# Optimization experiments

Measured on AMD Instinct MI355X. Metric: run time of the kernel, lower is better.

Reference implementation:

```python
import jax, jax.numpy as jnp
import numpy as np

B, S, D, H, DH = 8, 1024, 768, 12, 64
INIT_STD = 0.02
IGNORE = -100000.0


def setup_inputs() -> dict:
    key = jax.random.key(0)
    ks = jax.random.split(key, 5)
    return {
        "normalized_resid_pre": jax.random.normal(ks[0], (B, S, D), dtype=jnp.float32),
        "W_Q": jax.random.normal(ks[1], (H, D, DH), dtype=jnp.float32) * INIT_STD,
        "b_Q": jnp.zeros((H, DH), dtype=jnp.float32),
        "W_K": jax.random.normal(ks[2], (H, D, DH), dtype=jnp.float32) * INIT_STD,
        "b_K": jnp.zeros((H, DH), dtype=jnp.float32),
        "W_V": jax.random.normal(ks[3], (H, D, DH), dtype=jnp.float32) * INIT_STD,
        "b_V": jnp.zeros((H, DH), dtype=jnp.float32),
        "W_O": jax.random.normal(ks[4], (H, DH, D), dtype=jnp.float32) * INIT_STD,
        "b_O": jnp.zeros((D,), dtype=jnp.float32),
    }


def reference(normalized_resid_pre, W_Q, b_Q, W_K, b_K, W_V, b_V, W_O, b_O):
    x = normalized_resid_pre  # [B,S,D]
    q = jnp.einsum('bsd,hde->bshe', x, W_Q) + b_Q  # [B,S,H,DH]
    k = jnp.einsum('bsd,hde->bshe', x, W_K) + b_K
    v = jnp.einsum('bsd,hde->bshe', x, W_V) + b_V
    scores = jnp.einsum('bqhe,bkhe->bhqk', q, k) / jnp.sqrt(jnp.float32(DH))
    causal = jnp.triu(jnp.ones((S, S), dtype=bool), k=1)  # True above diagonal
    scores = jnp.where(causal, jnp.float32(IGNORE), scores)
    pattern = jax.nn.softmax(scores, axis=-1)  # [B,H,S,S]
    z = jnp.einsum('bhqk,bkhe->bqhe', pattern, v)  # [B,S,H,DH]
    attn_out = jnp.einsum('bqhe,hed->bqd', z, W_O) + b_O  # [B,S,D]
    return attn_out
```

## Files before the change

kernel.cpp:

```cpp
#include <hip/hip_runtime.h>
#include <hip/hip_bf16.h>
#include <stdint.h>

#define BB 8
#define SS 1024
#define DD 768
#define HH 12
#define DHH 64
#define BS (BB*SS)
#define NQKV (3*HH*DHH)

typedef __attribute__((ext_vector_type(8))) short bf16x8;
typedef __attribute__((ext_vector_type(4))) float f32x4;
typedef __attribute__((ext_vector_type(4))) unsigned int u32x4;

typedef const __attribute__((address_space(1))) unsigned int gu32;
typedef __attribute__((address_space(3))) unsigned int lu32;

static __device__ __forceinline__ unsigned short f2bf(float f) {
    union { float f; unsigned int u; } v; v.f = f;
    unsigned int u = v.u;
    unsigned int r = (u + 0x7fffu + ((u >> 16) & 1u)) >> 16;
    return (unsigned short)r;
}

static __device__ __forceinline__ unsigned int cvt_pk_bf16(float lo, float hi) {
    unsigned int r;
    asm("v_cvt_pk_bf16_f32 %0, %1, %2" : "=v"(r) : "v"(lo), "v"(hi));
    return r;
}


__global__ void k_f32_to_bf16(const float* __restrict__ in, unsigned short* __restrict__ out, int n) {
    int i = (blockIdx.x * 256 + threadIdx.x) * 4;
    if (i + 3 < n) {
        float4 v = *reinterpret_cast<const float4*>(in + i);
        ushort4 o;
        o.x = f2bf(v.x); o.y = f2bf(v.y); o.z = f2bf(v.z); o.w = f2bf(v.w);
        *reinterpret_cast<ushort4*>(out + i) = o;
    } else {
        for (; i < n; ++i) out[i] = f2bf(in[i]);
    }
}

__global__ void k_transpose_wqkv(const float* __restrict__ wq, const float* __restrict__ wk,
                                 const float* __restrict__ wv, unsigned short* __restrict__ wt) {
    __shared__ float tl[64][65];
    int rt = blockIdx.x;
    int z = blockIdx.y;
    int mat = z / 12, h = z - mat * 12;
    const float* src = ((mat == 0) ? wq : (mat == 1) ? wk : wv) + (size_t)h * 768 * 64;
    int d0 = rt * 64;
    int t = threadIdx.x;
    int row = t >> 4, c4 = (t & 15) * 4;
    #pragma unroll
    for (int p = 0; p < 4; ++p) {
        int d = p * 16 + row;
        float4 v = *reinterpret_cast<const float4*>(&src[(size_t)(d0 + d) * 64 + c4]);
        tl[d][c4 + 0] = v.x; tl[d][c4 + 1] = v.y; tl[d][c4 + 2] = v.z; tl[d][c4 + 3] = v.w;
    }
    __syncthreads();
    unsigned short* dstb = wt + ((size_t)(mat * 768 + h * 64)) * 768;
    #pragma unroll
    for (int p = 0; p < 4; ++p) {
        int e = p * 16 + row;
        ushort4 o;
        o.x = f2bf(tl[c4 + 0][e]); o.y = f2bf(tl[c4 + 1][e]);
        o.z = f2bf(tl[c4 + 2][e]); o.w = f2bf(tl[c4 + 3][e]);
        *reinterpret_cast<ushort4*>(&dstb[(size_t)e * 768 + d0 + c4]) = o;
    }
}

__global__ void k_transpose_wo(const float* __restrict__ wo, unsigned short* __restrict__ wot) {
    __shared__ float tl[64][65];
    int r0 = blockIdx.x * 64;
    int c0 = blockIdx.y * 64;
    int t = threadIdx.x;
    int row = t >> 4, c4 = (t & 15) * 4;
    #pragma unroll
    for (int p = 0; p < 4; ++p) {
        int r = p * 16 + row;
        float4 v = *reinterpret_cast<const float4*>(&wo[(size_t)(r0 + r) * 768 + c0 + c4]);
        tl[r][c4 + 0] = v.x; tl[r][c4 + 1] = v.y; tl[r][c4 + 2] = v.z; tl[r][c4 + 3] = v.w;
    }
    __syncthreads();
    #pragma unroll
    for (int p = 0; p < 4; ++p) {
        int c = p * 16 + row;
        ushort4 o;
        o.x = f2bf(tl[c4 + 0][c]); o.y = f2bf(tl[c4 + 1][c]);
        o.z = f2bf(tl[c4 + 2][c]); o.w = f2bf(tl[c4 + 3][c]);
        *reinterpret_cast<ushort4*>(&wot[(size_t)(c0 + c) * 768 + r0 + c4]) = o;
    }
}

__global__ void k_transpose_v(const unsigned short* __restrict__ vb, unsigned short* __restrict__ vtb) {
    __shared__ unsigned short tl[64][68];
    int s0 = blockIdx.x * 64;
    int bh = blockIdx.y;
    const unsigned short* src = vb + (size_t)bh * SS * DHH;
    unsigned short* dst = vtb + (size_t)bh * DHH * SS;
    int t = threadIdx.x;
    #pragma unroll
    for (int i = 0; i < 16; ++i) {
        int idx = t + i * 256;
        int sl = idx >> 6, e = idx & 63;
        tl[sl][e] = src[(size_t)(s0 + sl) * DHH + e];
    }
    __syncthreads();
    #pragma unroll
    for (int i = 0; i < 16; ++i) {
        int idx = t + i * 256;
        int e = idx >> 6, sl = idx & 63;
        dst[(size_t)e * SS + s0 + sl] = tl[sl][e];
    }
}


__launch_bounds__(256)
__global__ void k_gemm_qkv(const unsigned short* __restrict__ xb,
                           const unsigned short* __restrict__ wt,
                           const float* __restrict__ bq, const float* __restrict__ bk,
                           const float* __restrict__ bv,
                           unsigned short* __restrict__ qb,
                           unsigned short* __restrict__ kb,
                           unsigned short* __restrict__ vb) {
    __shared__ unsigned short As[128 * 32];
    __shared__ unsigned short Bs[128 * 32];
    int r0 = blockIdx.x * 128;
    int c0 = blockIdx.y * 128;
    int t = threadIdx.x;
    int w = t >> 6, l = t & 63;
    int lr = l & 15, lg = l >> 4;
    int wr = w >> 1, wc = w & 1;
    int srow = l >> 2, sko = (l & 3) * 8;

    f32x4 acc[4][4] = {};
    for (int k0 = 0; k0 < DD; k0 += 32) {
        __syncthreads();
        #pragma unroll
        for (int c = 0; c < 2; ++c) {
            int seg = w * 2 + c;
            int row = seg * 16 + srow;
            __builtin_amdgcn_global_load_lds(
                (gu32*)(xb + (size_t)(r0 + row) * DD + k0 + sko),
                (lu32*)&As[seg * 512], 16, 0, 0);
            __builtin_amdgcn_global_load_lds(
                (gu32*)(wt + (size_t)(c0 + row) * DD + k0 + sko),
                (lu32*)&Bs[seg * 512], 16, 0, 0);
        }
        __syncthreads();
        bf16x8 af[4], bfr[4];
        #pragma unroll
        for (int m = 0; m < 4; ++m)
            af[m] = *reinterpret_cast<const bf16x8*>(&As[(wr * 64 + m * 16 + lr) * 32 + lg * 8]);
        #pragma unroll
        for (int n = 0; n < 4; ++n)
            bfr[n] = *reinterpret_cast<const bf16x8*>(&Bs[(wc * 64 + n * 16 + lr) * 32 + lg * 8]);
        #pragma unroll
        for (int m = 0; m < 4; ++m)
            #pragma unroll
            for (int n = 0; n < 4; ++n)
                acc[m][n] = __builtin_amdgcn_mfma_f32_16x16x32_bf16(af[m], bfr[n], acc[m][n], 0, 0, 0);
    }
    #pragma unroll
    for (int n = 0; n < 4; ++n) {
        int c = c0 + wc * 64 + n * 16 + lr;
        int mat = c / 768;
        int within = c - mat * 768;
        int h = within >> 6, e = within & 63;
        const float* bptr = (mat == 0) ? bq : (mat == 1) ? bk : bv;
        float bias = bptr[within];
        unsigned short* dst = (mat == 0) ? qb : (mat == 1) ? kb : vb;
        #pragma unroll
        for (int m = 0; m < 4; ++m) {
            #pragma unroll
            for (int i = 0; i < 4; ++i) {
                int r = r0 + wr * 64 + m * 16 + lg * 4 + i;
                int b_ = r >> 10, s_ = r & 1023;
                dst[(((size_t)(b_ * HH + h)) * SS + s_) * DHH + e] = f2bf(acc[m][n][i] + bias);
            }
        }
    }
}


#define PW 34

__launch_bounds__(256, 3)
__global__ void k_attn(const unsigned short* __restrict__ qb,
                       const unsigned short* __restrict__ kb,
                       const unsigned short* __restrict__ vtb,
                       unsigned short* __restrict__ zb) {
    __shared__ unsigned short Ks[2][64 * 64];
    __shared__ unsigned short Vs[2][64 * 64];
    __shared__ unsigned int Pl[4][16 * PW];
    int id = blockIdx.x;
    int p = id / 96;
    int bh = id - p * 96;
    int qi = 15 - p;
    int q0 = qi * 64;

    int t = threadIdx.x, w = t >> 6, l = t & 63;
    int lr = l & 15, lg = l >> 4;
    const unsigned short* Qh = qb + (size_t)bh * SS * DHH;
    const unsigned short* Kh = kb + (size_t)bh * SS * DHH;
    const unsigned short* Vt = vtb + (size_t)bh * DHH * SS;
    int b_ = bh / HH, h = bh - b_ * HH;
    unsigned int* Pw = &Pl[w][0];

    int sr8 = l >> 3;
    int sc = ((l & 7) ^ sr8) * 8;

    auto STAGE = [&](int buf, int kbase) {
        #pragma unroll
        for (int c = 0; c < 2; ++c) {
            int seg = w * 2 + c;
            int row = seg * 8 + sr8;
            __builtin_amdgcn_global_load_lds(
                (gu32*)(Kh + (size_t)(kbase + row) * DHH + sc),
                (lu32*)&Ks[buf][seg * 512], 16, 0, 0);
            __builtin_amdgcn_global_load_lds(
                (gu32*)(Vt + (size_t)row * SS + kbase + sc),
                (lu32*)&Vs[buf][seg * 512], 16, 0, 0);
        }
    };

    int qabs = q0 + w * 16 + lr;
    STAGE(0, 0);
    bf16x8 qf[2];
    qf[0] = *reinterpret_cast<const bf16x8*>(Qh + (size_t)qabs * DHH + lg * 8);
    qf[1] = *reinterpret_cast<const bf16x8*>(Qh + (size_t)qabs * DHH + 32 + lg * 8);

    float m_r = -3.0e38f, l_r = 0.f;
    f32x4 zacc[4] = {};
    __syncthreads();

    for (int kt = 0; kt <= qi; ++kt) {
        int k0 = kt * 64;
        int cur = kt & 1;
        if (kt < qi) STAGE(cur ^ 1, k0 + 64);

        f32x4 sac[4] = {};
        #pragma unroll
        for (int ks = 0; ks < 2; ++ks) {
            #pragma unroll
            for (int ct = 0; ct < 4; ++ct) {
                bf16x8 kfr = *reinterpret_cast<const bf16x8*>(
                    &Ks[cur][(ct * 16 + lr) * 64 + (((ks * 4 + lg) ^ (lr & 7)) * 8)]);
                sac[ct] = __builtin_amdgcn_mfma_f32_16x16x32_bf16(kfr, qf[ks], sac[ct], 0, 0, 0);
            }
        }
        bool diag = (kt == qi);
        float sv[4][4];
        float pm = -3.0e38f;
        #pragma unroll
        for (int ct = 0; ct < 4; ++ct) {
            #pragma unroll
            for (int i = 0; i < 4; ++i) {
                float x = sac[ct][i] * 0.125f;
                if (diag) {
                    int kabs = k0 + ct * 16 + lg * 4 + i;
                    if (kabs > qabs) x = -3.0e38f;
                }
                sv[ct][i] = x;
                pm = fmaxf(pm, x);
            }
        }
        pm = fmaxf(pm, __shfl_xor(pm, 16));
        pm = fmaxf(pm, __shfl_xor(pm, 32));

        if (!__all(pm <= m_r + 8.f)) {
            float mn = fmaxf(m_r, pm);
            float alpha = __expf(m_r - mn);
            m_r = mn;
            l_r *= alpha;
            float aC[4];
            #pragma unroll
            for (int i = 0; i < 4; ++i) aC[i] = __shfl(alpha, lg * 4 + i);
            #pragma unroll
            for (int et = 0; et < 4; ++et)
                #pragma unroll
                for (int i = 0; i < 4; ++i) zacc[et][i] *= aC[i];
        }

        float ps = 0.f;
        #pragma unroll
        for (int ct = 0; ct < 4; ++ct) {
            float p0 = __expf(sv[ct][0] - m_r);
            float p1 = __expf(sv[ct][1] - m_r);
            float p2 = __expf(sv[ct][2] - m_r);
            float p3 = __expf(sv[ct][3] - m_r);
            ps += (p0 + p1) + (p2 + p3);
            unsigned int pk0 = cvt_pk_bf16(p0, p1);
            unsigned int pk1 = cvt_pk_bf16(p2, p3);
            *reinterpret_cast<uint2*>(&Pw[lr * PW + ct * 8 + lg * 2]) = make_uint2(pk0, pk1);
        }
        ps += __shfl_xor(ps, 16);
        ps += __shfl_xor(ps, 32);
        l_r += ps;

        #pragma unroll
        for (int ks = 0; ks < 2; ++ks) {
            bf16x8 pa = *reinterpret_cast<const bf16x8*>(&Pw[lr * PW + ks * 16 + lg * 4]);
            #pragma unroll
            for (int et = 0; et < 4; ++et) {
                bf16x8 vf = *reinterpret_cast<const bf16x8*>(
                    &Vs[cur][(et * 16 + lr) * 64 + (((ks * 4 + lg) ^ (lr & 7)) * 8)]);
                zacc[et] = __builtin_amdgcn_mfma_f32_16x16x32_bf16(pa, vf, zacc[et], 0, 0, 0);
            }
        }
        __syncthreads();
    }

    float lC[4];
    #pragma unroll
    for (int i = 0; i < 4; ++i) lC[i] = __shfl(l_r, lg * 4 + i);
    #pragma unroll
    for (int et = 0; et < 4; ++et) {
        #pragma unroll
        for (int i = 0; i < 4; ++i) {
            int r = q0 + w * 16 + lg * 4 + i;
            float z = zacc[et][i] / lC[i];
            zb[((size_t)(b_ * SS + r)) * DD + h * DHH + et * 16 + lr] = f2bf(z);
        }
    }
}


__launch_bounds__(256)
__global__ void k_gemm_out(const unsigned short* __restrict__ zb,
                           const unsigned short* __restrict__ wot,
                           const float* __restrict__ bo,
                           float* __restrict__ out) {
    __shared__ unsigned short As[128 * 32];
    __shared__ unsigned short Bs[128 * 32];
    int r0 = blockIdx.x * 128;
    int c0 = blockIdx.y * 128;
    int t = threadIdx.x;
    int w = t >> 6, l = t & 63;
    int lr = l & 15, lg = l >> 4;
    int wr = w >> 1, wc = w & 1;
    int srow = l >> 2, sko = (l & 3) * 8;

    f32x4 acc[4][4] = {};
    for (int k0 = 0; k0 < DD; k0 += 32) {
        __syncthreads();
        #pragma unroll
        for (int c = 0; c < 2; ++c) {
            int seg = w * 2 + c;
            int row = seg * 16 + srow;
            __builtin_amdgcn_global_load_lds(
                (gu32*)(zb + (size_t)(r0 + row) * DD + k0 + sko),
                (lu32*)&As[seg * 512], 16, 0, 0);
            __builtin_amdgcn_global_load_lds(
                (gu32*)(wot + (size_t)(c0 + row) * DD + k0 + sko),
                (lu32*)&Bs[seg * 512], 16, 0, 0);
        }
        __syncthreads();
        bf16x8 af[4], bfr[4];
        #pragma unroll
        for (int m = 0; m < 4; ++m)
            af[m] = *reinterpret_cast<const bf16x8*>(&As[(wr * 64 + m * 16 + lr) * 32 + lg * 8]);
        #pragma unroll
        for (int n = 0; n < 4; ++n)
            bfr[n] = *reinterpret_cast<const bf16x8*>(&Bs[(wc * 64 + n * 16 + lr) * 32 + lg * 8]);
        #pragma unroll
        for (int m = 0; m < 4; ++m)
            #pragma unroll
            for (int n = 0; n < 4; ++n)
                acc[m][n] = __builtin_amdgcn_mfma_f32_16x16x32_bf16(af[m], bfr[n], acc[m][n], 0, 0, 0);
    }
    #pragma unroll
    for (int n = 0; n < 4; ++n) {
        int c = c0 + wc * 64 + n * 16 + lr;
        float bias = bo[c];
        #pragma unroll
        for (int m = 0; m < 4; ++m) {
            #pragma unroll
            for (int i = 0; i < 4; ++i) {
                int r = r0 + wr * 64 + m * 16 + lg * 4 + i;
                out[(size_t)r * DD + c] = acc[m][n][i] + bias;
            }
        }
    }
}


extern "C" void kernel_launch(void* const* d_in, const int* in_sizes, int n_in,
                              void* d_out, int out_size, void* d_ws, size_t ws_size,
                              hipStream_t stream) {
    const float* x  = (const float*)d_in[0];
    const float* wq = (const float*)d_in[1];
    const float* bq = (const float*)d_in[2];
    const float* wk = (const float*)d_in[3];
    const float* bk = (const float*)d_in[4];
    const float* wv = (const float*)d_in[5];
    const float* bv = (const float*)d_in[6];
    const float* wo = (const float*)d_in[7];
    const float* bo = (const float*)d_in[8];
    float* out = (float*)d_out;

    char* ws = (char*)d_ws;
    size_t off = 0;
    auto alloc = [&](size_t bytes) -> char* {
        char* p = ws + off;
        off += (bytes + 255) & ~(size_t)255;
        return p;
    };
    unsigned short* xb   = (unsigned short*)alloc((size_t)BS * DD * 2);
    unsigned short* wt   = (unsigned short*)alloc((size_t)NQKV * DD * 2);
    unsigned short* wot  = (unsigned short*)alloc((size_t)DD * DD * 2);
    unsigned short* qb   = (unsigned short*)alloc((size_t)BB * HH * SS * DHH * 2);
    unsigned short* kb   = (unsigned short*)alloc((size_t)BB * HH * SS * DHH * 2);
    unsigned short* vb   = (unsigned short*)alloc((size_t)BB * HH * SS * DHH * 2);
    unsigned short* vtb  = (unsigned short*)alloc((size_t)BB * HH * SS * DHH * 2);
    unsigned short* zb   = (unsigned short*)alloc((size_t)BS * DD * 2);
    (void)ws_size; (void)in_sizes; (void)n_in; (void)out_size;

    k_f32_to_bf16<<<dim3((BS * DD) / (256 * 4)), dim3(256), 0, stream>>>(x, xb, BS * DD);
    k_transpose_wqkv<<<dim3(12, 36), dim3(256), 0, stream>>>(wq, wk, wv, wt);
    k_transpose_wo<<<dim3(12, 12), dim3(256), 0, stream>>>(wo, wot);
    k_gemm_qkv<<<dim3(BS / 128, NQKV / 128), dim3(256), 0, stream>>>(xb, wt, bq, bk, bv, qb, kb, vb);
    k_transpose_v<<<dim3(SS / 64, BB * HH), dim3(256), 0, stream>>>(vb, vtb);
    k_attn<<<dim3(16 * 96), dim3(256), 0, stream>>>(qb, kb, vtb, zb);
    k_gemm_out<<<dim3(BS / 128, DD / 128), dim3(256), 0, stream>>>(zb, wot, bo, out);
}
```

Before: 125.3 us.

## Double-buffer LDS tiles and swizzle K chunks in projection GEMMs

Both projection GEMMs (QKV and output) now use two LDS buffers. The next K tile is issued through global_load_lds while the current tile feeds the MFMAs, which overlaps global-memory latency with compute and drops one barrier per iteration. The 8-element K chunk each lane loads and reads is also permuted by row, an XOR-like swizzle meant to reduce LDS bank conflicts on the bf16x8 fragment reads. LDS use per block doubles, which may lower occupancy, and the correctness depends on the swizzle on the write side matching the read side.

```diff
diff --git a/kernel.cpp b/kernel.cpp
--- a/kernel.cpp
+++ b/kernel.cpp
@@ -125,43 +125,51 @@
                            unsigned short* __restrict__ qb,
                            unsigned short* __restrict__ kb,
                            unsigned short* __restrict__ vb) {
-    __shared__ unsigned short As[128 * 32];
-    __shared__ unsigned short Bs[128 * 32];
+    __shared__ unsigned short As[2][128 * 32];
+    __shared__ unsigned short Bs[2][128 * 32];
     int r0 = blockIdx.x * 128;
     int c0 = blockIdx.y * 128;
     int t = threadIdx.x;
     int w = t >> 6, l = t & 63;
     int lr = l & 15, lg = l >> 4;
     int wr = w >> 1, wc = w & 1;
-    int srow = l >> 2, sko = (l & 3) * 8;
-
-    f32x4 acc[4][4] = {};
-    for (int k0 = 0; k0 < DD; k0 += 32) {
-        __syncthreads();
+    int srow = l >> 2;
+    int g8 = (((l & 3) - (l >> 3)) & 3) * 8;
+
+    auto STAGE = [&](int buf, int k0) {
         #pragma unroll
         for (int c = 0; c < 2; ++c) {
             int seg = w * 2 + c;
             int row = seg * 16 + srow;
             __builtin_amdgcn_global_load_lds(
-                (gu32*)(xb + (size_t)(r0 + row) * DD + k0 + sko),
-                (lu32*)&As[seg * 512], 16, 0, 0);
-            __builtin_amdgcn_global_load_lds(
-                (gu32*)(wt + (size_t)(c0 + row) * DD + k0 + sko),
-                (lu32*)&Bs[seg * 512], 16, 0, 0);
-        }
-        __syncthreads();
+                (gu32*)(xb + (size_t)(r0 + row) * DD + k0 + g8),
+                (lu32*)&As[buf][seg * 512], 16, 0, 0);
+            __builtin_amdgcn_global_load_lds(
+                (gu32*)(wt + (size_t)(c0 + row) * DD + k0 + g8),
+                (lu32*)&Bs[buf][seg * 512], 16, 0, 0);
+        }
+    };
+
+    f32x4 acc[4][4] = {};
+    STAGE(0, 0);
+    __syncthreads();
+    int rdo = ((lg + (lr >> 1)) & 3) * 8;
+    for (int kk = 0; kk < 24; ++kk) {
+        int cur = kk & 1;
+        if (kk < 23) STAGE(cur ^ 1, kk * 32 + 32);
         bf16x8 af[4], bfr[4];
         #pragma unroll
         for (int m = 0; m < 4; ++m)
-            af[m] = *reinterpret_cast<const bf16x8*>(&As[(wr * 64 + m * 16 + lr) * 32 + lg * 8]);
+            af[m] = *reinterpret_cast<const bf16x8*>(&As[cur][(wr * 64 + m * 16 + lr) * 32 + rdo]);
         #pragma unroll
         for (int n = 0; n < 4; ++n)
-            bfr[n] = *reinterpret_cast<const bf16x8*>(&Bs[(wc * 64 + n * 16 + lr) * 32 + lg * 8]);
+            bfr[n] = *reinterpret_cast<const bf16x8*>(&Bs[cur][(wc * 64 + n * 16 + lr) * 32 + rdo]);
         #pragma unroll
         for (int m = 0; m < 4; ++m)
             #pragma unroll
             for (int n = 0; n < 4; ++n)
                 acc[m][n] = __builtin_amdgcn_mfma_f32_16x16x32_bf16(af[m], bfr[n], acc[m][n], 0, 0, 0);
+        __syncthreads();
     }
     #pragma unroll
     for (int n = 0; n < 4; ++n) {
@@ -333,43 +341,51 @@
                            const unsigned short* __restrict__ wot,
                            const float* __restrict__ bo,
                            float* __restrict__ out) {
-    __shared__ unsigned short As[128 * 32];
-    __shared__ unsigned short Bs[128 * 32];
+    __shared__ unsigned short As[2][128 * 32];
+    __shared__ unsigned short Bs[2][128 * 32];
     int r0 = blockIdx.x * 128;
     int c0 = blockIdx.y * 128;
     int t = threadIdx.x;
     int w = t >> 6, l = t & 63;
     int lr = l & 15, lg = l >> 4;
     int wr = w >> 1, wc = w & 1;
-    int srow = l >> 2, sko = (l & 3) * 8;
-
-    f32x4 acc[4][4] = {};
-    for (int k0 = 0; k0 < DD; k0 += 32) {
-        __syncthreads();
+    int srow = l >> 2;
+    int g8 = (((l & 3) - (l >> 3)) & 3) * 8;
+
+    auto STAGE = [&](int buf, int k0) {
         #pragma unroll
         for (int c = 0; c < 2; ++c) {
             int seg = w * 2 + c;
             int row = seg * 16 + srow;
             __builtin_amdgcn_global_load_lds(
-                (gu32*)(zb + (size_t)(r0 + row) * DD + k0 + sko),
-                (lu32*)&As[seg * 512], 16, 0, 0);
-            __builtin_amdgcn_global_load_lds(
-                (gu32*)(wot + (size_t)(c0 + row) * DD + k0 + sko),
-                (lu32*)&Bs[seg * 512], 16, 0, 0);
-        }
-        __syncthreads();
+                (gu32*)(zb + (size_t)(r0 + row) * DD + k0 + g8),
+                (lu32*)&As[buf][seg * 512], 16, 0, 0);
+            __builtin_amdgcn_global_load_lds(
+                (gu32*)(wot + (size_t)(c0 + row) * DD + k0 + g8),
+                (lu32*)&Bs[buf][seg * 512], 16, 0, 0);
+        }
+    };
+
+    f32x4 acc[4][4] = {};
+    STAGE(0, 0);
+    __syncthreads();
+    int rdo = ((lg + (lr >> 1)) & 3) * 8;
+    for (int kk = 0; kk < 24; ++kk) {
+        int cur = kk & 1;
+        if (kk < 23) STAGE(cur ^ 1, kk * 32 + 32);
         bf16x8 af[4], bfr[4];
         #pragma unroll
         for (int m = 0; m < 4; ++m)
-            af[m] = *reinterpret_cast<const bf16x8*>(&As[(wr * 64 + m * 16 + lr) * 32 + lg * 8]);
+            af[m] = *reinterpret_cast<const bf16x8*>(&As[cur][(wr * 64 + m * 16 + lr) * 32 + rdo]);
         #pragma unroll
         for (int n = 0; n < 4; ++n)
-            bfr[n] = *reinterpret_cast<const bf16x8*>(&Bs[(wc * 64 + n * 16 + lr) * 32 + lg * 8]);
+            bfr[n] = *reinterpret_cast<const bf16x8*>(&Bs[cur][(wc * 64 + n * 16 + lr) * 32 + rdo]);
         #pragma unroll
         for (int m = 0; m < 4; ++m)
             #pragma unroll
             for (int n = 0; n < 4; ++n)
                 acc[m][n] = __builtin_amdgcn_mfma_f32_16x16x32_bf16(af[m], bfr[n], acc[m][n], 0, 0, 0);
+        __syncthreads();
     }
     #pragma unroll
     for (int n = 0; n < 4; ++n) {
```

After: 133.4 us. 6.4% more time.
